# Performance work log

Measured on AMD Instinct MI355X. Metric: run time of the kernel, lower is better.

The kernel has to match this reference:

```python
import jax, jax.numpy as jnp
import numpy as np

N_STEPS = 2_097_152
DEPOL_RATE = 0.01


def _two_qubit_ops():
    sx = jnp.array([[0, 1], [1, 0]], dtype=jnp.complex64)
    sy = jnp.array([[0, -1j], [1j, 0]], dtype=jnp.complex64)
    sz = jnp.array([[1, 0], [0, -1]], dtype=jnp.complex64)
    eye2 = jnp.eye(2, dtype=jnp.complex64)
    # sigma (x|y|z) on qubit 1: sigma kron I
    return jnp.kron(sx, eye2), jnp.kron(sy, eye2), jnp.kron(sz, eye2)


def _target_unitary():
    # CNOT
    U = jnp.zeros((4, 4), dtype=jnp.complex64)
    return U.at[jnp.array([0, 1, 2, 3]), jnp.array([0, 1, 3, 2])].set(1.0)


def setup_inputs() -> dict:
    key = jax.random.key(0)
    pulses = jax.random.normal(key, (N_STEPS, 3), dtype=jnp.float32)
    dt = jnp.float32(5e-14)  # keeps per-step damping p = rate*dt*1e9 small but nonzero
    return {"pulses": pulses, "dt": dt}


def reference(pulses, dt):
    sx1, sy1, sz1 = _two_qubit_ops()
    U_target = _target_unitary()

    p = DEPOL_RATE * dt * 1e9  # depolarizing damping per step
    scale = (1.0 - p).astype(jnp.complex64)
    minus_i_dt = (-1j) * dt.astype(jnp.complex64)

    def step(U, pt):
        # H(t) = Ox sx1 + Oy sy1 + 0.5 * Delta sz1  (pt is [3] float32)
        H = pt[0] * sx1 + pt[1] * sy1 + (0.5 * pt[2]) * sz1
        U_new = scale * (U + minus_i_dt * (H @ U))
        return U_new, None

    U0 = jnp.eye(4, dtype=jnp.complex64)
    U, _ = jax.lax.scan(step, U0, pulses)

    # |tr(U_target^H U)|^2 / 16
    overlap = jnp.abs(jnp.sum(jnp.conj(U_target) * U)) ** 2
    fidelity = overlap / 16.0
    loss_phys = 1.0 - fidelity

    pulse_diff = pulses[1:] - pulses[:-1]
    reg_loss = jnp.mean(pulse_diff ** 2)
    total_loss = loss_phys + 0.01 * reg_loss
    return (total_loss, fidelity)
```

## Files before the change

kernel.cpp:

```cpp
#include <hip/hip_runtime.h>


#define N_STEPS 2097152
#define K1_BLOCKS 1024
#define K1_THREADS 256
#define TOTAL_THREADS (K1_BLOCKS * K1_THREADS)
#define STEPS_PER_THREAD (N_STEPS / TOTAL_THREADS)

struct C2 { double re, im; };

__device__ inline C2 cmul(C2 a, C2 b) {
    C2 r; r.re = a.re * b.re - a.im * b.im; r.im = a.re * b.im + a.im * b.re; return r;
}
__device__ inline C2 cadd(C2 a, C2 b) { C2 r; r.re = a.re + b.re; r.im = a.im + b.im; return r; }

__device__ inline void mat_mul(const double* L, const double* R, double* out) {
    C2 l00 = {L[0], L[1]}, l01 = {L[2], L[3]}, l10 = {L[4], L[5]}, l11 = {L[6], L[7]};
    C2 r00 = {R[0], R[1]}, r01 = {R[2], R[3]}, r10 = {R[4], R[5]}, r11 = {R[6], R[7]};
    C2 n00 = cadd(cmul(l00, r00), cmul(l01, r10));
    C2 n01 = cadd(cmul(l00, r01), cmul(l01, r11));
    C2 n10 = cadd(cmul(l10, r00), cmul(l11, r10));
    C2 n11 = cadd(cmul(l10, r01), cmul(l11, r11));
    out[0] = n00.re; out[1] = n00.im; out[2] = n01.re; out[3] = n01.im;
    out[4] = n10.re; out[5] = n10.im; out[6] = n11.re; out[7] = n11.im;
}

__device__ inline void wave_reduce_mat(double* m, double& reg) {
    const int lane = threadIdx.x & 63;
    #pragma unroll
    for (int off = 1; off < 64; off <<= 1) {
        double other[8];
        #pragma unroll
        for (int j = 0; j < 8; ++j) other[j] = __shfl_xor(m[j], off, 64);
        double tmp[8];
        if (lane & off) mat_mul(m, other, tmp);
        else            mat_mul(other, m, tmp);
        #pragma unroll
        for (int j = 0; j < 8; ++j) m[j] = tmp[j];
        reg += __shfl_xor(reg, off, 64);
    }
}

__global__ __launch_bounds__(K1_THREADS) void lindblad_partial_kernel(
    const float* __restrict__ pulses, const float* __restrict__ dt_ptr,
    double* __restrict__ ws) {
    const int tid = threadIdx.x;
    const int gid = blockIdx.x * K1_THREADS + tid;

    const float dtf = dt_ptr[0];
    const float pf = (0.01f * dtf) * 1e9f;
    const double s = (double)(1.0f - pf);
    const double dt = (double)dtf;
    const double sdt = s * dt;

    float arr[24];
    {
        const float4* p4 = (const float4*)(pulses + (size_t)gid * 24);
        #pragma unroll
        for (int j = 0; j < 6; ++j) {
            float4 v = p4[j];
            arr[4 * j + 0] = v.x; arr[4 * j + 1] = v.y;
            arr[4 * j + 2] = v.z; arr[4 * j + 3] = v.w;
        }
    }
    float nx = 0.f, ny = 0.f, nz = 0.f;
    const bool has_next = (gid < TOTAL_THREADS - 1);
    if (has_next) {
        const float* nxt = pulses + (size_t)(gid + 1) * 24;
        nx = nxt[0]; ny = nxt[1]; nz = nxt[2];
    }

    C2 p00 = {1.0, 0.0}, p01 = {0.0, 0.0}, p10 = {0.0, 0.0}, p11 = {1.0, 0.0};
    double reg = 0.0;

    #pragma unroll
    for (int k = 0; k < STEPS_PER_THREAD; ++k) {
        const double ox = (double)arr[3 * k + 0];
        const double oy = (double)arr[3 * k + 1];
        const double dl = (double)arr[3 * k + 2];

        C2 b00 = { s,         -0.5 * sdt * dl };
        C2 b01 = { -sdt * oy, -sdt * ox };
        C2 b10 = {  sdt * oy, -sdt * ox };
        C2 b11 = { s,          0.5 * sdt * dl };

        C2 n00 = cadd(cmul(b00, p00), cmul(b01, p10));
        C2 n01 = cadd(cmul(b00, p01), cmul(b01, p11));
        C2 n10 = cadd(cmul(b10, p00), cmul(b11, p10));
        C2 n11 = cadd(cmul(b10, p01), cmul(b11, p11));
        p00 = n00; p01 = n01; p10 = n10; p11 = n11;

        double dx, dy, dz;
        if (k < STEPS_PER_THREAD - 1) {
            dx = (double)arr[3 * k + 3] - ox;
            dy = (double)arr[3 * k + 4] - oy;
            dz = (double)arr[3 * k + 5] - dl;
            reg += dx * dx + dy * dy + dz * dz;
        } else if (has_next) {
            dx = (double)nx - ox; dy = (double)ny - oy; dz = (double)nz - dl;
            reg += dx * dx + dy * dy + dz * dz;
        }
    }

    double m[8] = {p00.re, p00.im, p01.re, p01.im, p10.re, p10.im, p11.re, p11.im};
    wave_reduce_mat(m, reg);

    __shared__ double wm[4][8];
    __shared__ double wr[4];
    const int wave = tid >> 6;
    if ((tid & 63) == 0) {
        #pragma unroll
        for (int j = 0; j < 8; ++j) wm[wave][j] = m[j];
        wr[wave] = reg;
    }
    __syncthreads();
    if (tid == 0) {
        double acc[8], tmp[8];
        #pragma unroll
        for (int j = 0; j < 8; ++j) acc[j] = wm[0][j];
        double r = wr[0];
        #pragma unroll
        for (int w = 1; w < 4; ++w) {
            mat_mul(wm[w], acc, tmp);
            #pragma unroll
            for (int j = 0; j < 8; ++j) acc[j] = tmp[j];
            r += wr[w];
        }
        double* out = ws + (size_t)blockIdx.x * 9;
        #pragma unroll
        for (int j = 0; j < 8; ++j) out[j] = acc[j];
        out[8] = r;
    }
}

#define K2_THREADS 256
#define PARTIALS_PER_THREAD (K1_BLOCKS / K2_THREADS)

__global__ __launch_bounds__(K2_THREADS) void lindblad_final_kernel(
    const double* __restrict__ ws, float* __restrict__ out) {
    const int tid = threadIdx.x;

    double acc[8] = {1.0, 0.0, 0.0, 0.0, 0.0, 0.0, 1.0, 0.0};
    double reg = 0.0;
    #pragma unroll
    for (int j = 0; j < PARTIALS_PER_THREAD; ++j) {
        const double* p = ws + (size_t)(tid * PARTIALS_PER_THREAD + j) * 9;
        double L[8], tmp[8];
        #pragma unroll
        for (int q = 0; q < 8; ++q) L[q] = p[q];
        mat_mul(L, acc, tmp);
        #pragma unroll
        for (int q = 0; q < 8; ++q) acc[q] = tmp[q];
        reg += p[8];
    }

    wave_reduce_mat(acc, reg);

    __shared__ double wm[4][8];
    __shared__ double wr[4];
    const int wave = tid >> 6;
    if ((tid & 63) == 0) {
        #pragma unroll
        for (int j = 0; j < 8; ++j) wm[wave][j] = acc[j];
        wr[wave] = reg;
    }
    __syncthreads();
    if (tid == 0) {
        double fin[8], tmp[8];
        #pragma unroll
        for (int j = 0; j < 8; ++j) fin[j] = wm[0][j];
        double r = wr[0];
        #pragma unroll
        for (int w = 1; w < 4; ++w) {
            mat_mul(wm[w], fin, tmp);
            #pragma unroll
            for (int j = 0; j < 8; ++j) fin[j] = tmp[j];
            r += wr[w];
        }
        const double p00r = fin[0], p00i = fin[1];
        const double tr_re = 2.0 * p00r, tr_im = 2.0 * p00i;
        const double fid = (tr_re * tr_re + tr_im * tr_im) / 16.0;
        const double reg_mean = r / (3.0 * (double)(N_STEPS - 1));
        const double total = (1.0 - fid) + 0.01 * reg_mean;
        out[0] = (float)total;
        out[1] = (float)fid;
    }
}

extern "C" void kernel_launch(void* const* d_in, const int* in_sizes, int n_in,
                              void* d_out, int out_size, void* d_ws, size_t ws_size,
                              hipStream_t stream) {
    const float* pulses = (const float*)d_in[0];
    const float* dt_ptr = (const float*)d_in[1];
    float* out = (float*)d_out;
    double* ws = (double*)d_ws;

    lindblad_partial_kernel<<<K1_BLOCKS, K1_THREADS, 0, stream>>>(pulses, dt_ptr, ws);
    lindblad_final_kernel<<<1, K2_THREADS, 0, stream>>>(ws, out);
}
```

Measured before the change: 80.04 us.

## Fuse final reduction into partial kernel via last-block atomic counter

Merges the two-kernel reduction into one kernel. Each block writes its partial matrix, fences, and bumps a global atomic counter, and the last block to arrive does the final ordered matrix-product reduction and writes the loss. This removes the second kernel launch and its dependency gap, but adds a memset on the stream and serialises the final combine onto whichever block finishes last. The wave reduction also swaps its divergent branch for select-based operand ordering.

```diff
diff --git a/kernel.cpp b/kernel.cpp
--- a/kernel.cpp
+++ b/kernel.cpp
@@ -6,6 +6,8 @@
 #define K1_THREADS 256
 #define TOTAL_THREADS (K1_BLOCKS * K1_THREADS)
 #define STEPS_PER_THREAD (N_STEPS / TOTAL_THREADS)
+#define PARTIAL_BYTES ((size_t)K1_BLOCKS * 9 * sizeof(double))
+#define FINAL_PER_THREAD (K1_BLOCKS / K1_THREADS)
 
 struct C2 { double re, im; };
 
@@ -29,21 +31,38 @@
     const int lane = threadIdx.x & 63;
     #pragma unroll
     for (int off = 1; off < 64; off <<= 1) {
-        double other[8];
+        const bool later = (lane & off) != 0;
+        double other[8], L[8], R[8], tmp[8];
         #pragma unroll
         for (int j = 0; j < 8; ++j) other[j] = __shfl_xor(m[j], off, 64);
-        double tmp[8];
-        if (lane & off) mat_mul(m, other, tmp);
-        else            mat_mul(other, m, tmp);
+        #pragma unroll
+        for (int j = 0; j < 8; ++j) { L[j] = later ? m[j] : other[j];
+                                      R[j] = later ? other[j] : m[j]; }
+        mat_mul(L, R, tmp);
         #pragma unroll
         for (int j = 0; j < 8; ++j) m[j] = tmp[j];
         reg += __shfl_xor(reg, off, 64);
     }
 }
 
-__global__ __launch_bounds__(K1_THREADS) void lindblad_partial_kernel(
+__device__ inline void combine4(double wm[4][8], double* wr, double* fin, double& r) {
+    double tmp[8];
+    #pragma unroll
+    for (int j = 0; j < 8; ++j) fin[j] = wm[0][j];
+    r = wr[0];
+    #pragma unroll
+    for (int w = 1; w < 4; ++w) {
+        mat_mul(wm[w], fin, tmp);
+        #pragma unroll
+        for (int j = 0; j < 8; ++j) fin[j] = tmp[j];
+        r += wr[w];
+    }
+}
+
+__global__ __launch_bounds__(K1_THREADS) void lindblad_fused_kernel(
     const float* __restrict__ pulses, const float* __restrict__ dt_ptr,
-    double* __restrict__ ws) {
+    double* __restrict__ ws, unsigned int* __restrict__ counter,
+    float* __restrict__ out) {
     const int tid = threadIdx.x;
     const int gid = blockIdx.x * K1_THREADS + tid;
 
@@ -90,14 +109,13 @@
         C2 n11 = cadd(cmul(b10, p01), cmul(b11, p11));
         p00 = n00; p01 = n01; p10 = n10; p11 = n11;
 
-        double dx, dy, dz;
         if (k < STEPS_PER_THREAD - 1) {
-            dx = (double)arr[3 * k + 3] - ox;
-            dy = (double)arr[3 * k + 4] - oy;
-            dz = (double)arr[3 * k + 5] - dl;
+            const double dx = (double)arr[3 * k + 3] - ox;
+            const double dy = (double)arr[3 * k + 4] - oy;
+            const double dz = (double)arr[3 * k + 5] - dl;
             reg += dx * dx + dy * dy + dz * dz;
         } else if (has_next) {
-            dx = (double)nx - ox; dy = (double)ny - oy; dz = (double)nz - dl;
+            const double dx = (double)nx - ox, dy = (double)ny - oy, dz = (double)nz - dl;
             reg += dx * dx + dy * dy + dz * dz;
         }
     }
@@ -107,6 +125,7 @@
 
     __shared__ double wm[4][8];
     __shared__ double wr[4];
+    __shared__ int sh_last;
     const int wave = tid >> 6;
     if ((tid & 63) == 0) {
         #pragma unroll
@@ -114,73 +133,52 @@
         wr[wave] = reg;
     }
     __syncthreads();
+
     if (tid == 0) {
-        double acc[8], tmp[8];
-        #pragma unroll
-        for (int j = 0; j < 8; ++j) acc[j] = wm[0][j];
-        double r = wr[0];
-        #pragma unroll
-        for (int w = 1; w < 4; ++w) {
-            mat_mul(wm[w], acc, tmp);
-            #pragma unroll
-            for (int j = 0; j < 8; ++j) acc[j] = tmp[j];
-            r += wr[w];
-        }
-        double* out = ws + (size_t)blockIdx.x * 9;
-        #pragma unroll
-        for (int j = 0; j < 8; ++j) out[j] = acc[j];
-        out[8] = r;
-    }
-}
-
-#define K2_THREADS 256
-#define PARTIALS_PER_THREAD (K1_BLOCKS / K2_THREADS)
-
-__global__ __launch_bounds__(K2_THREADS) void lindblad_final_kernel(
-    const double* __restrict__ ws, float* __restrict__ out) {
-    const int tid = threadIdx.x;
+        double acc[8]; double r;
+        combine4(wm, wr, acc, r);
+        double* o = ws + (size_t)blockIdx.x * 9;
+        #pragma unroll
+        for (int j = 0; j < 8; ++j) o[j] = acc[j];
+        o[8] = r;
+        __threadfence();
+        unsigned int old = atomicAdd(counter, 1u);
+        sh_last = (old == K1_BLOCKS - 1) ? 1 : 0;
+    }
+    __syncthreads();
+    if (!sh_last) return;
+
+    __threadfence();
 
     double acc[8] = {1.0, 0.0, 0.0, 0.0, 0.0, 0.0, 1.0, 0.0};
-    double reg = 0.0;
-    #pragma unroll
-    for (int j = 0; j < PARTIALS_PER_THREAD; ++j) {
-        const double* p = ws + (size_t)(tid * PARTIALS_PER_THREAD + j) * 9;
+    double r = 0.0;
+    #pragma unroll
+    for (int j = 0; j < FINAL_PER_THREAD; ++j) {
+        const double* p = ws + (size_t)(tid * FINAL_PER_THREAD + j) * 9;
         double L[8], tmp[8];
         #pragma unroll
         for (int q = 0; q < 8; ++q) L[q] = p[q];
         mat_mul(L, acc, tmp);
         #pragma unroll
         for (int q = 0; q < 8; ++q) acc[q] = tmp[q];
-        reg += p[8];
-    }
-
-    wave_reduce_mat(acc, reg);
-
-    __shared__ double wm[4][8];
-    __shared__ double wr[4];
-    const int wave = tid >> 6;
+        r += p[8];
+    }
+
+    wave_reduce_mat(acc, r);
+
+    __syncthreads();
     if ((tid & 63) == 0) {
         #pragma unroll
         for (int j = 0; j < 8; ++j) wm[wave][j] = acc[j];
-        wr[wave] = reg;
+        wr[wave] = r;
     }
     __syncthreads();
     if (tid == 0) {
-        double fin[8], tmp[8];
-        #pragma unroll
-        for (int j = 0; j < 8; ++j) fin[j] = wm[0][j];
-        double r = wr[0];
-        #pragma unroll
-        for (int w = 1; w < 4; ++w) {
-            mat_mul(wm[w], fin, tmp);
-            #pragma unroll
-            for (int j = 0; j < 8; ++j) fin[j] = tmp[j];
-            r += wr[w];
-        }
-        const double p00r = fin[0], p00i = fin[1];
-        const double tr_re = 2.0 * p00r, tr_im = 2.0 * p00i;
+        double fin[8]; double rr;
+        combine4(wm, wr, fin, rr);
+        const double tr_re = 2.0 * fin[0], tr_im = 2.0 * fin[1];
         const double fid = (tr_re * tr_re + tr_im * tr_im) / 16.0;
-        const double reg_mean = r / (3.0 * (double)(N_STEPS - 1));
+        const double reg_mean = rr / (3.0 * (double)(N_STEPS - 1));
         const double total = (1.0 - fid) + 0.01 * reg_mean;
         out[0] = (float)total;
         out[1] = (float)fid;
@@ -194,7 +192,9 @@
     const float* dt_ptr = (const float*)d_in[1];
     float* out = (float*)d_out;
     double* ws = (double*)d_ws;
-
-    lindblad_partial_kernel<<<K1_BLOCKS, K1_THREADS, 0, stream>>>(pulses, dt_ptr, ws);
-    lindblad_final_kernel<<<1, K2_THREADS, 0, stream>>>(ws, out);
-}
+    unsigned int* counter = (unsigned int*)((char*)d_ws + PARTIAL_BYTES);
+
+    hipMemsetAsync(counter, 0, sizeof(unsigned int), stream);
+    lindblad_fused_kernel<<<K1_BLOCKS, K1_THREADS, 0, stream>>>(
+        pulses, dt_ptr, ws, counter, out);
+}
```

After: 93.78 us. 1.17x slower.
